# Kernel tuning notes

Measured on AMD Instinct MI355X. Metric: run time of the kernel, lower is better.

Reference implementation:

```python
import jax, jax.numpy as jnp
import numpy as np

EMBED_DIM = 1024
NUM_HEADS = 16
HEAD_DIM = EMBED_DIM // NUM_HEADS
B, T = 4, 2048


def setup_inputs() -> dict:
    key = jax.random.key(0)
    ks = jax.random.split(key, 10)
    s = 1.0 / np.sqrt(EMBED_DIM)
    inp = {
        "x": jax.random.normal(ks[0], (B, T, EMBED_DIM), dtype=jnp.float32),
        "mask": jnp.ones((B, T), dtype=bool),
        "q_w": jax.random.uniform(ks[1], (EMBED_DIM, EMBED_DIM), jnp.float32, -s, s),
        "q_b": jax.random.uniform(ks[2], (EMBED_DIM,), jnp.float32, -s, s),
        "k_w": jax.random.uniform(ks[3], (EMBED_DIM, EMBED_DIM), jnp.float32, -s, s),
        "k_b": jax.random.uniform(ks[4], (EMBED_DIM,), jnp.float32, -s, s),
        "v_w": jax.random.uniform(ks[5], (EMBED_DIM, EMBED_DIM), jnp.float32, -s, s),
        "v_b": jax.random.uniform(ks[6], (EMBED_DIM,), jnp.float32, -s, s),
        "o_w": jax.random.uniform(ks[7], (EMBED_DIM, EMBED_DIM), jnp.float32, -s, s),
        "o_b": jax.random.uniform(ks[8], (EMBED_DIM,), jnp.float32, -s, s),
    }
    return inp


def reference(x, mask, q_w, q_b, k_w, k_b, v_w, v_b, o_w, o_b):
    # NOTE: original module accepts `mask` but never uses it; dropout defined but never applied.
    Bn, Tn, C = x.shape
    H, D = NUM_HEADS, HEAD_DIM
    # Linear: x @ W.T + b, then split heads -> [B, H, T, D]
    Q = (x @ q_w.T + q_b).reshape(Bn, Tn, H, D).transpose(0, 2, 1, 3)
    K = (x @ k_w.T + k_b).reshape(Bn, Tn, H, D).transpose(0, 2, 1, 3)
    V = (x @ v_w.T + v_b).reshape(Bn, Tn, H, D).transpose(0, 2, 1, 3)
    scores = jnp.einsum("bhqd,bhkd->bhqk", Q, K) / jnp.sqrt(jnp.float32(D))
    attn = jax.nn.softmax(scores, axis=-1)
    out = jnp.einsum("bhqk,bhkd->bhqd", attn, V)
    out = out.transpose(0, 2, 1, 3).reshape(Bn, Tn, C)
    return out @ o_w.T + o_b
```

## Files before the change

### kernel.cpp

```cpp
#include <hip/hip_runtime.h>
#include <stdint.h>

#define B_ 4
#define T_ 2048
#define C_ 1024
#define H_ 16
#define D_ 64

typedef __attribute__((ext_vector_type(8))) short bf8;
typedef __attribute__((ext_vector_type(4))) float f4;

__device__ __forceinline__ ushort f2bf(float f) {
  union { float f; uint32_t u; } c; c.f = f;
  uint32_t u = c.u;
  uint32_t r = (u + 0x7fffu + ((u >> 16) & 1u)) >> 16;
  return (ushort)r;
}

__device__ __forceinline__ uint32_t cvtpk(float a, float b) {
  uint32_t r;
  asm("v_cvt_pk_bf16_f32 %0, %1, %2" : "=v"(r) : "v"(a), "v"(b));
  return r;
}

__global__ __launch_bounds__(256) void cast_f32_bf16(const float* __restrict__ in,
                                                     ushort* __restrict__ out, int n) {
  int i = (blockIdx.x * 256 + threadIdx.x) * 4;
  if (i >= n) return;
  float4 v = *(const float4*)(in + i);
  ushort4 o;
  o.x = f2bf(v.x); o.y = f2bf(v.y); o.z = f2bf(v.z); o.w = f2bf(v.w);
  *(ushort4*)(out + i) = o;
}

__global__ __launch_bounds__(256) void cast4_w(const float* __restrict__ w0,
                                               const float* __restrict__ w1,
                                               const float* __restrict__ w2,
                                               const float* __restrict__ w3,
                                               ushort* __restrict__ o0,
                                               ushort* __restrict__ o1,
                                               ushort* __restrict__ o2,
                                               ushort* __restrict__ o3) {
  const float* in;
  ushort* out;
  switch (blockIdx.y) {
    case 0: in = w0; out = o0; break;
    case 1: in = w1; out = o1; break;
    case 2: in = w2; out = o2; break;
    default: in = w3; out = o3; break;
  }
  int i = (blockIdx.x * 256 + threadIdx.x) * 4;
  float4 v = *(const float4*)(in + i);
  ushort4 o;
  o.x = f2bf(v.x); o.y = f2bf(v.y); o.z = f2bf(v.z); o.w = f2bf(v.w);
  *(ushort4*)(out + i) = o;
}

__global__ __launch_bounds__(256) void transpose_v(const ushort* __restrict__ in,
                                                   ushort* __restrict__ out) {
  __shared__ ushort tile[64 * 65];
  const int tid = threadIdx.x;
  const int bh = blockIdx.y, t0 = blockIdx.x * 64;
  const int r = tid >> 3, c8 = (tid & 7) * 8;

  const ushort* src = in + ((size_t)bh * T_ + t0 + r) * D_ + c8;
  *(int4*)&tile[r * 65 + c8]        = *(const int4*)&src[0];
  *(int4*)&tile[(r + 32) * 65 + c8] = *(const int4*)&src[32 * D_];
  __syncthreads();

#pragma unroll
  for (int p = 0; p < 2; ++p) {
    int d = p * 32 + (tid >> 3), tc = (tid & 7) * 8;
    ushort tmp[8];
#pragma unroll
    for (int i = 0; i < 8; ++i) tmp[i] = tile[(tc + i) * 65 + d];
    *(int4*)&out[((size_t)bh * D_ + d) * T_ + t0 + tc] = *(int4*)tmp;
  }
}

#define BM 128
#define BN 128
#define BK 32

__global__ __launch_bounds__(256) void gemm_bt(const ushort* __restrict__ A,
                                               const ushort* __restrict__ W,
                                               const float* __restrict__ b0,
                                               const float* __restrict__ b1,
                                               const float* __restrict__ b2,
                                               void* __restrict__ outp,
                                               int K, int mode, float qsc) {
  __shared__ ushort As[2][BM * BK];
  __shared__ ushort Bs[2][BN * BK];
  const int tid = threadIdx.x;
  const int w = tid >> 6, l = tid & 63, lo = l & 15, hi = l >> 4;
  const int wr = (w >> 1) * 64, wc = (w & 1) * 64;

  const int i = blockIdx.x;
  const int m0 = ((i & 7) * 8 + ((i >> 3) & 7)) * BM;
  const int n0 = (i >> 6) * BN;

  f4 acc[4][4];
#pragma unroll
  for (int ii = 0; ii < 4; ++ii)
#pragma unroll
    for (int j = 0; j < 4; ++j) acc[ii][j] = (f4){0.f, 0.f, 0.f, 0.f};

  const int r0 = tid >> 2;
  const int kk = (tid & 3) * 8;
  const ushort* Ag  = A + (size_t)(m0 + r0) * K + kk;
  const ushort* Ag2 = A + (size_t)(m0 + 64 + r0) * K + kk;
  const ushort* Wg  = W + (size_t)(n0 + r0) * K + kk;
  const ushort* Wg2 = W + (size_t)(n0 + 64 + r0) * K + kk;

#define GSTAGE(bb, k0)                                                                             \
  {                                                                                                \
    __builtin_amdgcn_global_load_lds((const __attribute__((address_space(1))) void*)(Ag + (k0)),   \
                                     (__attribute__((address_space(3))) void*)&As[bb][tid * 8], 16, 0, 0);  \
    __builtin_amdgcn_global_load_lds((const __attribute__((address_space(1))) void*)(Ag2 + (k0)),  \
                                     (__attribute__((address_space(3))) void*)&As[bb][2048 + tid * 8], 16, 0, 0); \
    __builtin_amdgcn_global_load_lds((const __attribute__((address_space(1))) void*)(Wg + (k0)),   \
                                     (__attribute__((address_space(3))) void*)&Bs[bb][tid * 8], 16, 0, 0);  \
    __builtin_amdgcn_global_load_lds((const __attribute__((address_space(1))) void*)(Wg2 + (k0)),  \
                                     (__attribute__((address_space(3))) void*)&Bs[bb][2048 + tid * 8], 16, 0, 0); \
  }

  GSTAGE(0, 0);
  __syncthreads();
  int cur = 0;

  for (int k0 = 0; k0 < K; k0 += BK) {
    if (k0 + BK < K) GSTAGE(cur ^ 1, k0 + BK);

    bf8 af[4], bfr[4];
#pragma unroll
    for (int mt = 0; mt < 4; ++mt)
      af[mt] = *(const bf8*)&As[cur][(wr + mt * 16 + lo) * BK + hi * 8];
#pragma unroll
    for (int nt = 0; nt < 4; ++nt)
      bfr[nt] = *(const bf8*)&Bs[cur][(wc + nt * 16 + lo) * BK + hi * 8];
#pragma unroll
    for (int mt = 0; mt < 4; ++mt)
#pragma unroll
      for (int nt = 0; nt < 4; ++nt)
        acc[mt][nt] = __builtin_amdgcn_mfma_f32_16x16x32_bf16(af[mt], bfr[nt], acc[mt][nt], 0, 0, 0);

    __syncthreads();
    cur ^= 1;
  }
#undef GSTAGE

  if (mode == 0) {
    float* O = (float*)outp;
#pragma unroll
    for (int mt = 0; mt < 4; ++mt)
#pragma unroll
      for (int nt = 0; nt < 4; ++nt) {
        int n = n0 + wc + nt * 16 + lo;
        float bv = b0[n];
#pragma unroll
        for (int j = 0; j < 4; ++j) {
          int m = m0 + wr + mt * 16 + hi * 4 + j;
          O[(size_t)m * C_ + n] = acc[mt][nt][j] + bv;
        }
      }
  } else {
    const int proj = n0 >> 10;
    const float* bp = (proj == 0) ? b0 : ((proj == 1) ? b1 : b2);
    const float os = (proj == 0) ? qsc : 1.0f;
    ushort* O = (ushort*)outp + (size_t)proj * (8u << 20);
#pragma unroll
    for (int mt = 0; mt < 4; ++mt)
#pragma unroll
      for (int nt = 0; nt < 4; ++nt) {
        int n = n0 + wc + nt * 16 + lo;
        int nl = n & 1023;
        int h = nl >> 6, d = n & 63;
        float bv = bp[nl];
#pragma unroll
        for (int j = 0; j < 4; ++j) {
          int m = m0 + wr + mt * 16 + hi * 4 + j;
          int b = m >> 11, t = m & 2047;
          O[(size_t)((b << 4) + h) * (T_ * D_) + t * D_ + d] = f2bf((acc[mt][nt][j] + bv) * os);
        }
      }
  }
}

__global__ __launch_bounds__(256, 2) void attn_kernel(const ushort* __restrict__ Q,
                                                      const ushort* __restrict__ Kg,
                                                      const ushort* __restrict__ VT,
                                                      ushort* __restrict__ O) {
  __shared__ ushort Ks[2][64 * 64];
  __shared__ ushort Vs[2][64 * 64];

  const int tid = threadIdx.x;
  const int w = tid >> 6, l = tid & 63, lo = l & 15, hi = l >> 4;
  const int bh = blockIdx.y;
  const int q0 = blockIdx.x * 256 + w * 64;
  const ushort* Qb  = Q  + (size_t)bh * T_ * D_;
  const ushort* Kb  = Kg + (size_t)bh * T_ * D_;
  const ushort* VTb = VT + (size_t)bh * D_ * T_;

  bf8 qf[4][2];
#pragma unroll
  for (int qs = 0; qs < 4; ++qs)
#pragma unroll
    for (int c = 0; c < 2; ++c)
      qf[qs][c] = *(const bf8*)&Qb[(q0 + qs * 16 + lo) * D_ + c * 32 + hi * 8];

  f4 o[4][4];
#pragma unroll
  for (int qs = 0; qs < 4; ++qs)
#pragma unroll
    for (int dt = 0; dt < 4; ++dt) o[qs][dt] = (f4){0.f, 0.f, 0.f, 0.f};
  float Lloc[4] = {0.f, 0.f, 0.f, 0.f};

  const int rowA  = tid >> 3;
  const int colsw = ((tid & 7) ^ (rowA & 7)) * 8;
  const int permA = ((rowA >> 2) & 3) * 8 + ((rowA >> 4) & 1) * 4 + (rowA & 3);
  const ushort* Ksrc0 = Kb  + (size_t)permA * D_ + colsw;
  const ushort* Ksrc1 = Kb  + (size_t)(32 + permA) * D_ + colsw;
  const ushort* Vsrc0 = VTb + (size_t)rowA * T_ + colsw;
  const ushort* Vsrc1 = VTb + (size_t)(rowA + 32) * T_ + colsw;

  const int swz = (lo & 7) << 3;
  const int NT = T_ / 64;

#define STAGE(b, kvo)                                                                              \
  {                                                                                                \
    __builtin_amdgcn_global_load_lds((const __attribute__((address_space(1))) void*)(Ksrc0 + (size_t)(kvo) * D_), \
                                     (__attribute__((address_space(3))) void*)&Ks[b][tid * 8], 16, 0, 0);          \
    __builtin_amdgcn_global_load_lds((const __attribute__((address_space(1))) void*)(Ksrc1 + (size_t)(kvo) * D_), \
                                     (__attribute__((address_space(3))) void*)&Ks[b][2048 + tid * 8], 16, 0, 0);   \
    __builtin_amdgcn_global_load_lds((const __attribute__((address_space(1))) void*)(Vsrc0 + (kvo)),               \
                                     (__attribute__((address_space(3))) void*)&Vs[b][tid * 8], 16, 0, 0);          \
    __builtin_amdgcn_global_load_lds((const __attribute__((address_space(1))) void*)(Vsrc1 + (kvo)),               \
                                     (__attribute__((address_space(3))) void*)&Vs[b][2048 + tid * 8], 16, 0, 0);   \
  }

  STAGE(0, 0);
  __syncthreads();
  int cur = 0;

  for (int t = 0; t < NT; ++t) {
    if (t + 1 < NT) STAGE(cur ^ 1, (t + 1) * 64);

    const ushort* Kc = &Ks[cur][0];
    const ushort* Vc = &Vs[cur][0];

    bf8 kf[4][2], vf[4][2];
#pragma unroll
    for (int n = 0; n < 4; ++n) {
      kf[n][0] = *(const bf8*)&Kc[(n * 16 + lo) * 64 + ((hi * 8) ^ swz)];
      kf[n][1] = *(const bf8*)&Kc[(n * 16 + lo) * 64 + ((32 + hi * 8) ^ swz)];
    }
#pragma unroll
    for (int dt = 0; dt < 4; ++dt) {
      vf[dt][0] = *(const bf8*)&Vc[(dt * 16 + lo) * 64 + ((hi * 8) ^ swz)];
      vf[dt][1] = *(const bf8*)&Vc[(dt * 16 + lo) * 64 + ((32 + hi * 8) ^ swz)];
    }

#pragma unroll
    for (int qs = 0; qs < 4; ++qs) {
      f4 z[4];
#pragma unroll
      for (int n = 0; n < 4; ++n) {
        f4 zz = (f4){0.f, 0.f, 0.f, 0.f};
        zz = __builtin_amdgcn_mfma_f32_16x16x32_bf16(kf[n][0], qf[qs][0], zz, 0, 0, 0);
        zz = __builtin_amdgcn_mfma_f32_16x16x32_bf16(kf[n][1], qf[qs][1], zz, 0, 0, 0);
        z[n] = zz;
      }

      uint32_t pd[8];
      float ls = 0.f;
#pragma unroll
      for (int n = 0; n < 4; ++n) {
        float e0 = __builtin_amdgcn_exp2f(z[n][0]);
        float e1 = __builtin_amdgcn_exp2f(z[n][1]);
        float e2 = __builtin_amdgcn_exp2f(z[n][2]);
        float e3 = __builtin_amdgcn_exp2f(z[n][3]);
        ls += (e0 + e1) + (e2 + e3);
        pd[n * 2 + 0] = cvtpk(e0, e1);
        pd[n * 2 + 1] = cvtpk(e2, e3);
      }
      Lloc[qs] += ls;
      union U8 { uint32_t u[4]; bf8 v; } u0, u1;
      u0.u[0] = pd[0]; u0.u[1] = pd[1]; u0.u[2] = pd[2]; u0.u[3] = pd[3];
      u1.u[0] = pd[4]; u1.u[1] = pd[5]; u1.u[2] = pd[6]; u1.u[3] = pd[7];

#pragma unroll
      for (int dt = 0; dt < 4; ++dt) {
        o[qs][dt] = __builtin_amdgcn_mfma_f32_16x16x32_bf16(u0.v, vf[dt][0], o[qs][dt], 0, 0, 0);
        o[qs][dt] = __builtin_amdgcn_mfma_f32_16x16x32_bf16(u1.v, vf[dt][1], o[qs][dt], 0, 0, 0);
      }
    }

    __syncthreads();
    cur ^= 1;
  }
#undef STAGE

  const int b = bh >> 4, h = bh & 15;
#pragma unroll
  for (int qs = 0; qs < 4; ++qs) {
    float Ltot = Lloc[qs];
    Ltot += __shfl_xor(Ltot, 16);
    Ltot += __shfl_xor(Ltot, 32);
#pragma unroll
    for (int j = 0; j < 4; ++j) {
      float invL = 1.0f / __shfl(Ltot, hi * 4 + j);
      int q = q0 + qs * 16 + hi * 4 + j;
#pragma unroll
      for (int dt = 0; dt < 4; ++dt)
        O[(size_t)(b * T_ + q) * C_ + h * D_ + dt * 16 + lo] = f2bf(o[qs][dt][j] * invL);
    }
  }
}

extern "C" void kernel_launch(void* const* d_in, const int* in_sizes, int n_in,
                              void* d_out, int out_size, void* d_ws, size_t ws_size,
                              hipStream_t stream) {
  const float* x  = (const float*)d_in[0];
  const float* qw = (const float*)d_in[2];
  const float* qb = (const float*)d_in[3];
  const float* kw = (const float*)d_in[4];
  const float* kb = (const float*)d_in[5];
  const float* vw = (const float*)d_in[6];
  const float* vb = (const float*)d_in[7];
  const float* ow = (const float*)d_in[8];
  const float* ob = (const float*)d_in[9];
  float* out = (float*)d_out;

  char* ws = (char*)d_ws;
  ushort* xbf   = (ushort*)ws;
  ushort* VTws  = (ushort*)ws;
  ushort* qwbf  = (ushort*)(ws + (16u << 20));
  ushort* kwbf  = qwbf + (1u << 20);
  ushort* vwbf  = kwbf + (1u << 20);
  ushort* owbf  = vwbf + (1u << 20);
  ushort* Qws   = (ushort*)(ws + (24u << 20));
  ushort* attnw = (ushort*)(ws + (72u << 20));
  ushort* Vws   = (ushort*)(ws + (56u << 20));

  const int NX = B_ * T_ * C_;
  const int NW = C_ * C_;
  cast_f32_bf16<<<NX / 4 / 256, 256, 0, stream>>>(x, xbf, NX);
  cast4_w<<<dim3(NW / 4 / 256, 4), 256, 0, stream>>>(qw, kw, vw, ow, qwbf, kwbf, vwbf, owbf);

  const float QSC = 0.125f * 1.44269504f;
  gemm_bt<<<1536, 256, 0, stream>>>(xbf, qwbf, qb, kb, vb, Qws, C_, 1, QSC);

  transpose_v<<<dim3(T_ / 64, B_ * H_), 256, 0, stream>>>(Vws, VTws);

  attn_kernel<<<dim3(T_ / 256, B_ * H_), 256, 0, stream>>>(Qws, Qws + (size_t)(8u << 20), VTws, attnw);

  gemm_bt<<<512, 256, 0, stream>>>(attnw, owbf, ob, nullptr, nullptr, out, C_, 0, 1.0f);
}
```

Before: 201.3 us.

## Replace GEMM with 256x256-tile 8-wave kernel using swizzled LDS and phased pipeline

Replaces the 128x128x32 double-buffered GEMM with a 256x256x64 tile kernel run by 512 threads (8 waves, each 128x64). It uses XOR-swizzled LDS layout, 128KB dynamic shared memory, split staging with fine-grained vmcnt waits and barriers, and s_setprio around MFMA bursts. The aim is higher arithmetic intensity per block and more overlap of loads with MFMA for the QKV and output projections. In exchange it launches far fewer blocks (384 and 128), which leaves many CUs idle on the output projection, and it uses heavy register and LDS per block.

```diff
diff --git a/kernel.cpp b/kernel.cpp
--- a/kernel.cpp
+++ b/kernel.cpp
@@ -6,6 +6,7 @@
 #define C_ 1024
 #define H_ 16
 #define D_ 64
+#define CK 1024
 
 typedef __attribute__((ext_vector_type(8))) short bf8;
 typedef __attribute__((ext_vector_type(4))) float f4;
@@ -78,89 +79,123 @@
   }
 }
 
-#define BM 128
-#define BN 128
-#define BK 32
-
-__global__ __launch_bounds__(256) void gemm_bt(const ushort* __restrict__ A,
-                                               const ushort* __restrict__ W,
-                                               const float* __restrict__ b0,
-                                               const float* __restrict__ b1,
-                                               const float* __restrict__ b2,
-                                               void* __restrict__ outp,
-                                               int K, int mode, float qsc) {
-  __shared__ ushort As[2][BM * BK];
-  __shared__ ushort Bs[2][BN * BK];
+__global__ __launch_bounds__(512, 2) void gemm8(const ushort* __restrict__ A,
+                                                const ushort* __restrict__ W,
+                                                const float* __restrict__ b0,
+                                                const float* __restrict__ b1,
+                                                const float* __restrict__ b2,
+                                                void* __restrict__ outp,
+                                                int mode, float qsc) {
+  extern __shared__ ushort smem[];
+  ushort* sA = smem;
+  ushort* sB = smem + 32768;
+
   const int tid = threadIdx.x;
   const int w = tid >> 6, l = tid & 63, lo = l & 15, hi = l >> 4;
-  const int wr = (w >> 1) * 64, wc = (w & 1) * 64;
+  const int wm = w >> 2, wn = w & 3;
 
   const int i = blockIdx.x;
-  const int m0 = ((i & 7) * 8 + ((i >> 3) & 7)) * BM;
-  const int n0 = (i >> 6) * BN;
-
-  f4 acc[4][4];
-#pragma unroll
-  for (int ii = 0; ii < 4; ++ii)
-#pragma unroll
-    for (int j = 0; j < 4; ++j) acc[ii][j] = (f4){0.f, 0.f, 0.f, 0.f};
-
-  const int r0 = tid >> 2;
-  const int kk = (tid & 3) * 8;
-  const ushort* Ag  = A + (size_t)(m0 + r0) * K + kk;
-  const ushort* Ag2 = A + (size_t)(m0 + 64 + r0) * K + kk;
-  const ushort* Wg  = W + (size_t)(n0 + r0) * K + kk;
-  const ushort* Wg2 = W + (size_t)(n0 + 64 + r0) * K + kk;
-
-#define GSTAGE(bb, k0)                                                                             \
-  {                                                                                                \
-    __builtin_amdgcn_global_load_lds((const __attribute__((address_space(1))) void*)(Ag + (k0)),   \
-                                     (__attribute__((address_space(3))) void*)&As[bb][tid * 8], 16, 0, 0);  \
-    __builtin_amdgcn_global_load_lds((const __attribute__((address_space(1))) void*)(Ag2 + (k0)),  \
-                                     (__attribute__((address_space(3))) void*)&As[bb][2048 + tid * 8], 16, 0, 0); \
-    __builtin_amdgcn_global_load_lds((const __attribute__((address_space(1))) void*)(Wg + (k0)),   \
-                                     (__attribute__((address_space(3))) void*)&Bs[bb][tid * 8], 16, 0, 0);  \
-    __builtin_amdgcn_global_load_lds((const __attribute__((address_space(1))) void*)(Wg2 + (k0)),  \
-                                     (__attribute__((address_space(3))) void*)&Bs[bb][2048 + tid * 8], 16, 0, 0); \
-  }
-
-  GSTAGE(0, 0);
-  __syncthreads();
+  const int m0 = ((i & 7) * 4 + ((i >> 3) & 3)) * 256;
+  const int n0 = (i >> 5) * 256;
+
+  const int rl = tid >> 3, c7 = tid & 7;
+  const int scol = (c7 ^ (rl & 7)) * 8;
+  const ushort* Asrc = A + (size_t)(m0 + rl) * CK + scol;
+  const ushort* Bsrc = W + (size_t)(n0 + (tid >> 8) * 64 + (rl & 31)) * CK + scol;
+  const int Bd0 = (tid >> 8) * 4096 + (rl & 31) * 64 + c7 * 8;
+
+  const int sw0 = (hi ^ (lo & 7)) * 8;
+  const int sw1 = ((4 + hi) ^ (lo & 7)) * 8;
+  const int arow = wm * 128 + lo;
+  const int brow = wn * 64 + lo;
+
+  f4 acc[8][4];
+#pragma unroll
+  for (int f = 0; f < 8; ++f)
+#pragma unroll
+    for (int g = 0; g < 4; ++g) acc[f][g] = (f4){0.f, 0.f, 0.f, 0.f};
+
+#define GL(src, dst) __builtin_amdgcn_global_load_lds(                                   \
+      (const __attribute__((address_space(1))) void*)(src),                              \
+      (__attribute__((address_space(3))) void*)(dst), 16, 0, 0)
+#define STG_A(nb, mh, kn) {                                                              \
+    GL(Asrc + (kn) + (size_t)((mh) * 64) * CK,       &sA[(nb)*16384 + (mh)*4096 + tid*8]);        \
+    GL(Asrc + (kn) + (size_t)((mh) * 64 + 128) * CK, &sA[(nb)*16384 + 8192 + (mh)*4096 + tid*8]); }
+#define STG_B(nb, nh, kn) {                                                              \
+    GL(Bsrc + (kn) + (size_t)((nh) * 32) * CK,       &sB[(nb)*16384 + (nh)*2048 + Bd0]);          \
+    GL(Bsrc + (kn) + (size_t)((nh) * 32 + 128) * CK, &sB[(nb)*16384 + 8192 + (nh)*2048 + Bd0]); }
+#define VMC(s)  asm volatile("s_waitcnt vmcnt(" s ")" ::: "memory")
+#define PH_BAR  { __builtin_amdgcn_s_barrier(); asm volatile("" ::: "memory"); }
+#define LDA(cb, mh) {                                                                    \
+  _Pragma("unroll")                                                                      \
+  for (int f = 0; f < 4; ++f) {                                                          \
+    af[f][0] = *(const bf8*)&sA[(cb)*16384 + (arow + (mh)*64 + f*16)*64 + sw0];          \
+    af[f][1] = *(const bf8*)&sA[(cb)*16384 + (arow + (mh)*64 + f*16)*64 + sw1]; } }
+#define LDB(cb, dst, nh) {                                                               \
+  _Pragma("unroll")                                                                      \
+  for (int g = 0; g < 2; ++g) {                                                          \
+    dst[g][0] = *(const bf8*)&sB[(cb)*16384 + (brow + (nh)*32 + g*16)*64 + sw0];         \
+    dst[g][1] = *(const bf8*)&sB[(cb)*16384 + (brow + (nh)*32 + g*16)*64 + sw1]; } }
+#define MM(fo, go, bfr) {                                                                \
+  __builtin_amdgcn_s_setprio(1);                                                         \
+  _Pragma("unroll")                                                                      \
+  for (int f = 0; f < 4; ++f)                                                            \
+    _Pragma("unroll")                                                                    \
+    for (int g = 0; g < 2; ++g) {                                                        \
+      acc[(fo)+f][(go)+g] = __builtin_amdgcn_mfma_f32_16x16x32_bf16(af[f][0], bfr[g][0], acc[(fo)+f][(go)+g], 0, 0, 0); \
+      acc[(fo)+f][(go)+g] = __builtin_amdgcn_mfma_f32_16x16x32_bf16(af[f][1], bfr[g][1], acc[(fo)+f][(go)+g], 0, 0, 0); } \
+  __builtin_amdgcn_s_setprio(0); }
+
+  bf8 af[4][2], bA[2][2], bB[2][2];
+
+  STG_A(0, 0, 0); STG_A(0, 1, 0); STG_B(0, 0, 0); STG_B(0, 1, 0);
+  VMC("0"); PH_BAR;
   int cur = 0;
 
-  for (int k0 = 0; k0 < K; k0 += BK) {
-    if (k0 + BK < K) GSTAGE(cur ^ 1, k0 + BK);
-
-    bf8 af[4], bfr[4];
-#pragma unroll
-    for (int mt = 0; mt < 4; ++mt)
-      af[mt] = *(const bf8*)&As[cur][(wr + mt * 16 + lo) * BK + hi * 8];
-#pragma unroll
-    for (int nt = 0; nt < 4; ++nt)
-      bfr[nt] = *(const bf8*)&Bs[cur][(wc + nt * 16 + lo) * BK + hi * 8];
-#pragma unroll
-    for (int mt = 0; mt < 4; ++mt)
-#pragma unroll
-      for (int nt = 0; nt < 4; ++nt)
-        acc[mt][nt] = __builtin_amdgcn_mfma_f32_16x16x32_bf16(af[mt], bfr[nt], acc[mt][nt], 0, 0, 0);
-
-    __syncthreads();
-    cur ^= 1;
-  }
-#undef GSTAGE
+  for (int t = 0; t < (CK / 64) - 1; ++t) {
+    const int nb = cur ^ 1;
+    const int kn = (t + 1) * 64;
+    LDA(cur, 0); LDB(cur, bA, 0);
+    STG_A(nb, 0, kn); STG_B(nb, 0, kn);
+    VMC("6"); PH_BAR;
+    MM(0, 0, bA); PH_BAR;
+    LDB(cur, bB, 1);
+    STG_B(nb, 1, kn);
+    VMC("6"); PH_BAR;
+    MM(0, 2, bB); PH_BAR;
+    LDA(cur, 1);
+    STG_A(nb, 1, kn);
+    VMC("4"); PH_BAR;
+    MM(4, 0, bA); PH_BAR;
+    MM(4, 2, bB); PH_BAR;
+    cur = nb;
+  }
+  VMC("0"); PH_BAR;
+  LDA(cur, 0); LDB(cur, bA, 0); MM(0, 0, bA);
+  LDB(cur, bB, 1);              MM(0, 2, bB);
+  LDA(cur, 1);                  MM(4, 0, bA);
+                                MM(4, 2, bB);
+#undef GL
+#undef STG_A
+#undef STG_B
+#undef VMC
+#undef PH_BAR
+#undef LDA
+#undef LDB
+#undef MM
 
   if (mode == 0) {
     float* O = (float*)outp;
 #pragma unroll
-    for (int mt = 0; mt < 4; ++mt)
-#pragma unroll
-      for (int nt = 0; nt < 4; ++nt) {
-        int n = n0 + wc + nt * 16 + lo;
+    for (int f = 0; f < 8; ++f)
+#pragma unroll
+      for (int gn = 0; gn < 4; ++gn) {
+        int n = n0 + wn * 64 + gn * 16 + lo;
         float bv = b0[n];
 #pragma unroll
         for (int j = 0; j < 4; ++j) {
-          int m = m0 + wr + mt * 16 + hi * 4 + j;
-          O[(size_t)m * C_ + n] = acc[mt][nt][j] + bv;
+          int m = m0 + wm * 128 + f * 16 + hi * 4 + j;
+          O[(size_t)m * C_ + n] = acc[f][gn][j] + bv;
         }
       }
   } else {
@@ -169,18 +204,18 @@
     const float os = (proj == 0) ? qsc : 1.0f;
     ushort* O = (ushort*)outp + (size_t)proj * (8u << 20);
 #pragma unroll
-    for (int mt = 0; mt < 4; ++mt)
-#pragma unroll
-      for (int nt = 0; nt < 4; ++nt) {
-        int n = n0 + wc + nt * 16 + lo;
+    for (int f = 0; f < 8; ++f)
+#pragma unroll
+      for (int gn = 0; gn < 4; ++gn) {
+        int n = n0 + wn * 64 + gn * 16 + lo;
         int nl = n & 1023;
         int h = nl >> 6, d = n & 63;
         float bv = bp[nl];
 #pragma unroll
         for (int j = 0; j < 4; ++j) {
-          int m = m0 + wr + mt * 16 + hi * 4 + j;
+          int m = m0 + wm * 128 + f * 16 + hi * 4 + j;
           int b = m >> 11, t = m & 2047;
-          O[(size_t)((b << 4) + h) * (T_ * D_) + t * D_ + d] = f2bf((acc[mt][nt][j] + bv) * os);
+          O[(size_t)((b << 4) + h) * (T_ * D_) + t * D_ + d] = f2bf((acc[f][gn][j] + bv) * os);
         }
       }
   }
@@ -339,8 +374,10 @@
   ushort* vwbf  = kwbf + (1u << 20);
   ushort* owbf  = vwbf + (1u << 20);
   ushort* Qws   = (ushort*)(ws + (24u << 20));
+  ushort* Vws   = (ushort*)(ws + (56u << 20));
   ushort* attnw = (ushort*)(ws + (72u << 20));
-  ushort* Vws   = (ushort*)(ws + (56u << 20));
+
+  hipFuncSetAttribute((const void*)gemm8, hipFuncAttributeMaxDynamicSharedMemorySize, 131072);
 
   const int NX = B_ * T_ * C_;
   const int NW = C_ * C_;
@@ -348,11 +385,11 @@
   cast4_w<<<dim3(NW / 4 / 256, 4), 256, 0, stream>>>(qw, kw, vw, ow, qwbf, kwbf, vwbf, owbf);
 
   const float QSC = 0.125f * 1.44269504f;
-  gemm_bt<<<1536, 256, 0, stream>>>(xbf, qwbf, qb, kb, vb, Qws, C_, 1, QSC);
+  gemm8<<<384, 512, 131072, stream>>>(xbf, qwbf, qb, kb, vb, Qws, 1, QSC);
 
   transpose_v<<<dim3(T_ / 64, B_ * H_), 256, 0, stream>>>(Vws, VTws);
 
   attn_kernel<<<dim3(T_ / 256, B_ * H_), 256, 0, stream>>>(Qws, Qws + (size_t)(8u << 20), VTws, attnw);
 
-  gemm_bt<<<512, 256, 0, stream>>>(attnw, owbf, ob, nullptr, nullptr, out, C_, 0, 1.0f);
-}
+  gemm8<<<128, 512, 131072, stream>>>(attnw, owbf, ob, nullptr, nullptr, out, 0, 1.0f);
+}
```

Result: faster. 189.0 us (-6.1%).
